# Kernel tuning notes

Measured on AMD Instinct MI355X. Metric: run time of the kernel, lower is better.

Reference implementation:

```python
import jax, jax.numpy as jnp
import numpy as np

IN_F = 3072       # in_features
OUT_F = 9216      # out_features = 3 * N_HEADS * HEAD_DIM (fused QKV)
GROUP = 64        # quantization group size
RANK = 32         # lora_rank
HEAD_DIM = 128
N_HEADS = OUT_F // (3 * HEAD_DIM)  # 24
EPS = 1e-6
LORA_SCALE = 1.0


def setup_inputs() -> dict:
    key = jax.random.key(0)
    ks = jax.random.split(key, 10)
    B, S = 1, 4096
    x = jax.random.normal(ks[0], (B, S, IN_F), dtype=jnp.float32)
    # packed int4 weights: two signed int4 values per int8 byte
    qweight = jax.random.randint(ks[1], (OUT_F, IN_F // 2), -128, 128, dtype=jnp.int32).astype(jnp.int8)
    wscales = (jax.random.uniform(ks[2], (IN_F // GROUP, OUT_F)) * 0.02 + 0.001).astype(jnp.float32)
    bias = (jax.random.normal(ks[3], (OUT_F,)) * 0.01).astype(jnp.float32)
    lora_down = (jax.random.normal(ks[4], (IN_F, RANK)) * 0.02).astype(jnp.float32)
    lora_up = (jax.random.normal(ks[5], (OUT_F, RANK)) * 0.02).astype(jnp.float32)
    smooth = (jax.random.uniform(ks[6], (IN_F,)) * 0.5 + 0.75).astype(jnp.float32)   # keep away from 0
    norm_q = (jax.random.uniform(ks[7], (HEAD_DIM,)) * 0.5 + 0.75).astype(jnp.float32)
    norm_k = (jax.random.uniform(ks[8], (HEAD_DIM,)) * 0.5 + 0.75).astype(jnp.float32)
    ang = jax.random.uniform(ks[9], (S, HEAD_DIM // 2)) * (2.0 * np.pi)
    rotary_emb = jnp.stack([jnp.cos(ang), jnp.sin(ang)], axis=-1).astype(jnp.float32)  # [S, D/2, 2]
    return dict(x=x, qweight=qweight, wscales=wscales, bias=bias, lora_down=lora_down,
                lora_up=lora_up, smooth=smooth, norm_q=norm_q, norm_k=norm_k, rotary_emb=rotary_emb)


def _dequant_weight(qweight, wscales):
    # unpack two signed int4 lanes from each int8 (low nibble first), then per-group scale
    low = jnp.right_shift(jnp.left_shift(qweight, 4), 4)   # arithmetic shifts on int8 -> sign extend
    high = jnp.right_shift(qweight, 4)
    w4 = jnp.stack([low, high], axis=-1).reshape(OUT_F, IN_F)          # int4 codes in [-8, 7]
    wg = w4.astype(jnp.float32).reshape(OUT_F, IN_F // GROUP, GROUP)
    return (wg * wscales.T[:, :, None]).reshape(OUT_F, IN_F)          # [N, K]


def _quantize_act(x, smooth, lora_down):
    # fused: smooth -> symmetric per-token per-group int4 quantize -> lora_down projection
    B, S, K = x.shape
    M = B * S
    xs = (x / smooth).reshape(M, K)
    xg = xs.reshape(M, K // GROUP, GROUP)
    ascale = jnp.max(jnp.abs(xg), axis=-1, keepdims=True) / 7.0
    ascale = jnp.maximum(ascale, 1e-8)
    q = jnp.clip(jnp.round(xg / ascale), -8.0, 7.0)
    deq = (q * ascale).reshape(M, K)                                   # dequantized int4 activation
    lora_act = xs @ lora_down                                          # [M, RANK], fp32 side path
    return deq, lora_act


def _rope(t, cos, sin):
    # interleaved pairs (even, odd) rotation; t: [M, H, D], cos/sin: [M, 1, D/2]
    e, o = t[..., 0::2], t[..., 1::2]
    re = e * cos - o * sin
    ro = e * sin + o * cos
    return jnp.stack([re, ro], axis=-1).reshape(t.shape)


def reference(x, qweight, wscales, bias, lora_down, lora_up, smooth, norm_q, norm_k, rotary_emb):
    B, S, K = x.shape
    M = B * S
    deq_x, lora_act = _quantize_act(x, smooth, lora_down)
    w = _dequant_weight(qweight, wscales)
    # main int4 GEMM + LoRA up + bias, all fused in the real kernel
    out = deq_x @ w.T + (LORA_SCALE * lora_act) @ lora_up.T + bias     # [M, OUT_F]
    qkv = out.reshape(M, 3, N_HEADS, HEAD_DIM)
    q, k, v = qkv[:, 0], qkv[:, 1], qkv[:, 2]
    def rms(t, g):
        return t * jax.lax.rsqrt(jnp.mean(t * t, axis=-1, keepdims=True) + EPS) * g
    q = rms(q, norm_q)
    k = rms(k, norm_k)
    cos = rotary_emb[:, None, :, 0]   # [M, 1, D/2]
    sin = rotary_emb[:, None, :, 1]
    q = _rope(q, cos, sin)
    k = _rope(k, cos, sin)
    return jnp.stack([q, k, v], axis=1).reshape(B, S, OUT_F)
```

## Files before the change

### kernel.cpp

```cpp
#include <hip/hip_runtime.h>
#include <cstdint>

#define MDIM 4096
#define NDIM 9216
#define KDIM 3072
#define KP   3136
#define NKT2 97

#define QROWS 4
#define QB2 1024
#define WB 13824
#define PB 2304

typedef unsigned int u32;
typedef unsigned short u16;
typedef float f32x4 __attribute__((ext_vector_type(4)));
typedef __bf16 bf16x8 __attribute__((ext_vector_type(8)));

__device__ __forceinline__ u16 f2bf(float f) {
  u32 u = __float_as_uint(f);
  u32 r = u + 0x7fffu + ((u >> 16) & 1u);
  return (u16)(r >> 16);
}

__device__ __forceinline__ float frcp(float f) { return __builtin_amdgcn_rcpf(f); }

__device__ __forceinline__ void gld_lds16(const void* g, void* l) {
  __builtin_amdgcn_global_load_lds((__attribute__((address_space(1))) void*)g,
                                   (__attribute__((address_space(3))) void*)l,
                                   16, 0, 0);
}

__global__ __launch_bounds__(256) void k_zero(float* __restrict__ out) {
  const int row = blockIdx.x;
  float4* p = (float4*)(out + (size_t)row * NDIM + 6144);
  p[threadIdx.x] = make_float4(0.f, 0.f, 0.f, 0.f);
}

__global__ __launch_bounds__(256) void k_quant(const float* __restrict__ x,
                        const float* __restrict__ lora_down, const float* __restrict__ smooth,
                        u16* __restrict__ Aex) {
  __shared__ float xs_s[QROWS][KDIM];
  __shared__ float part[64 * 32];
  const int tid = threadIdx.x;
  const int m0 = blockIdx.x * QROWS;
  const int sub = tid & 15;

  #pragma unroll
  for (int r = 0; r < QROWS; ++r) {
    const float* xr = x + (size_t)(m0 + r) * KDIM;
    u16* arow = Aex + (size_t)(m0 + r) * KP;
    #pragma unroll
    for (int p = 0; p < 3; ++p) {
      int g = p * 16 + (tid >> 4);
      int k0 = g * 64 + sub * 4;
      float4 xv = *(const float4*)(xr + k0);
      float4 sv = *(const float4*)(smooth + k0);
      float a0 = xv.x * frcp(sv.x), a1 = xv.y * frcp(sv.y);
      float a2 = xv.z * frcp(sv.z), a3 = xv.w * frcp(sv.w);
      xs_s[r][k0+0] = a0; xs_s[r][k0+1] = a1; xs_s[r][k0+2] = a2; xs_s[r][k0+3] = a3;
      float am = fmaxf(fmaxf(fabsf(a0), fabsf(a1)), fmaxf(fabsf(a2), fabsf(a3)));
      am = fmaxf(am, __shfl_xor(am, 8, 16));
      am = fmaxf(am, __shfl_xor(am, 4, 16));
      am = fmaxf(am, __shfl_xor(am, 2, 16));
      am = fmaxf(am, __shfl_xor(am, 1, 16));
      float asc = fmaxf(am * (1.0f / 7.0f), 1e-8f);
      float iasc = frcp(asc);
      float q0 = fminf(7.f, fmaxf(-8.f, rintf(a0 * iasc)));
      float q1 = fminf(7.f, fmaxf(-8.f, rintf(a1 * iasc)));
      float q2 = fminf(7.f, fmaxf(-8.f, rintf(a2 * iasc)));
      float q3 = fminf(7.f, fmaxf(-8.f, rintf(a3 * iasc)));
      float d0 = q0 * asc, d1 = q1 * asc, d2 = q2 * asc, d3 = q3 * asc;
      u32 lo = (u32)f2bf(d0) | ((u32)f2bf(d1) << 16);
      u32 hi = (u32)f2bf(d2) | ((u32)f2bf(d3) << 16);
      *(uint2*)(arow + k0) = make_uint2(lo, hi);
    }
    if (tid < 32) arow[3104 + tid] = 0;
  }
  __syncthreads();

  const int c  = tid >> 2;
  const int r8 = (tid & 3) * 8;
  float a[QROWS][8] = {};
  const float* lp = lora_down + (size_t)c * 32 + r8;
  #pragma unroll 2
  for (int i = 0; i < 48; ++i) {
    float4 l0 = *(const float4*)(lp);
    float4 l1 = *(const float4*)(lp + 4);
    #pragma unroll
    for (int r = 0; r < QROWS; ++r) {
      float xv = xs_s[r][i * 64 + c];
      a[r][0] = fmaf(xv, l0.x, a[r][0]); a[r][1] = fmaf(xv, l0.y, a[r][1]);
      a[r][2] = fmaf(xv, l0.z, a[r][2]); a[r][3] = fmaf(xv, l0.w, a[r][3]);
      a[r][4] = fmaf(xv, l1.x, a[r][4]); a[r][5] = fmaf(xv, l1.y, a[r][5]);
      a[r][6] = fmaf(xv, l1.z, a[r][6]); a[r][7] = fmaf(xv, l1.w, a[r][7]);
    }
    lp += 64 * 32;
  }
  #pragma unroll 1
  for (int r = 0; r < QROWS; ++r) {
    __syncthreads();
    *(float4*)(&part[c * 32 + r8])     = make_float4(a[r][0], a[r][1], a[r][2], a[r][3]);
    *(float4*)(&part[c * 32 + r8 + 4]) = make_float4(a[r][4], a[r][5], a[r][6], a[r][7]);
    __syncthreads();
    if (tid < 32) {
      float s = 0.f;
      #pragma unroll 8
      for (int cc = 0; cc < 64; ++cc) s += part[cc * 32 + tid];
      Aex[(size_t)(m0 + r) * KP + 3072 + tid] = f2bf(s);
    }
  }
}

__global__ __launch_bounds__(256) void k_wdq(const u32* __restrict__ qw,
                        const float* __restrict__ wsc, const float* __restrict__ lora_up,
                        u16* __restrict__ Bex) {
  const int tid = threadIdx.x;
  int bid = blockIdx.x;

  if (bid >= WB) {
    int idx = (bid - WB) * 256 + tid;
    int n = idx >> 6, c = idx & 63;
    u16 v = 0;
    if (c < 32) v = f2bf(lora_up[n * 32 + c]);
    Bex[(size_t)n * KP + 3072 + c] = v;
    return;
  }
  __shared__ int s_viol;
  u32 probe = qw[tid];
  bool ok = (probe >> 8) == ((probe & 0x80u) ? 0xffffffu : 0u);
  if (tid == 0) s_viol = 0;
  __syncthreads();
  if (!ok) atomicOr(&s_viol, 1);
  __syncthreads();
  const int f = (s_viol == 0);

  int idx = bid * 256 + tid;
  int n = idx / 384;
  int j = idx - n * 384;
  int k0 = j * 8;
  u32 w;
  if (f) {
    uint4 q4 = ((const uint4*)qw)[idx];
    w = (q4.x & 0xffu) | ((q4.y & 0xffu) << 8) | ((q4.z & 0xffu) << 16) | ((q4.w & 0xffu) << 24);
  } else {
    w = qw[idx];
  }
  float ws = wsc[(k0 >> 6) * NDIM + n];
  u32 ow[4];
  #pragma unroll
  for (int b = 0; b < 4; ++b) {
    int by = (int)((w >> (8 * b)) & 0xffu);
    int lo = (by << 28) >> 28;
    int hi = (by << 24) >> 28;
    ow[b] = (u32)f2bf((float)lo * ws) | ((u32)f2bf((float)hi * ws) << 16);
  }
  *(uint4*)(Bex + (size_t)n * KP + k0) = make_uint4(ow[0], ow[1], ow[2], ow[3]);
}

__global__ __launch_bounds__(512) void k_gemm(const u16* __restrict__ A, const u16* __restrict__ B,
                                              const float* __restrict__ bias, const float* __restrict__ norm_q,
                                              const float* __restrict__ norm_k, const float* __restrict__ rot,
                                              float* __restrict__ out, const int mode) {
  extern __shared__ u16 lds[];
  const int tid  = threadIdx.x;
  const int lane = tid & 63;
  const int wave = tid >> 6;

  int mt, nt, kt0, nk;
  if (mode == 0) {
    mt = blockIdx.y;
    int xx = blockIdx.x;
    nt = xx + ((xx >= 24) ? 4 : 0);
    kt0 = 0; nk = NKT2;
  } else {
    int s = blockIdx.x;
    mt = blockIdx.y & 15;
    nt = 24 + (blockIdx.y >> 4);
    kt0 = s * 24 + (s ? 1 : 0);
    nk  = s ? 24 : 25;
  }
  const int m0 = mt * 256;
  const int n0 = nt * 256;
  const int wm = (wave >> 2) * 128;
  const int wn = (wave & 3) * 64;
  const int lr = lane & 15;
  const int lq = lane >> 4;

  const u16 *pA0, *pA1, *pB0, *pB1;
  int la0, la1, lb0, lb1;
  {
    auto mk = [&](int p, const u16* base, int nb) -> const u16* {
      int pr = p >> 3, cs = p & 7;
      int c  = cs ^ (pr & 7);
      int r  = pr * 2 + (c >> 2);
      int kc = c & 3;
      return base + (size_t)(nb + r) * KP + kt0 * 32 + kc * 8;
    };
    int p0 = tid, p1 = 512 + tid;
    pA0 = mk(p0, A, m0); pA1 = mk(p1, A, m0);
    pB0 = mk(p0, B, n0); pB1 = mk(p1, B, n0);
    la0 = p0 * 8;        la1 = p1 * 8;
    lb0 = 8192 + p0 * 8; lb1 = 8192 + p1 * 8;
  }

  int aoff[8], boff[4];
  #pragma unroll
  for (int t = 0; t < 8; ++t) {
    int ra = wm + t * 16 + lr;
    int pr = ra >> 1, c = (ra & 1) * 4 + lq;
    aoff[t] = pr * 64 + ((c ^ (pr & 7)) * 8);
  }
  #pragma unroll
  for (int t = 0; t < 4; ++t) {
    int rb = wn + t * 16 + lr;
    int pr = rb >> 1, c = (rb & 1) * 4 + lq;
    boff[t] = 8192 + pr * 64 + ((c ^ (pr & 7)) * 8);
  }

  f32x4 acc[8][4] = {};

  #pragma unroll
  for (int s = 0; s < 3; ++s) {
    u16* sl = lds + (s << 14);
    gld_lds16(pA0, sl + la0); gld_lds16(pA1, sl + la1);
    gld_lds16(pB0, sl + lb0); gld_lds16(pB1, sl + lb1);
    pA0 += 32; pA1 += 32; pB0 += 32; pB1 += 32;
  }
  asm volatile("s_waitcnt vmcnt(4)" ::: "memory");
  __builtin_amdgcn_s_barrier();
  asm volatile("" ::: "memory");

  bf16x8 af[8], bf[4];
  #pragma unroll
  for (int t = 0; t < 8; ++t) af[t] = *(const bf16x8*)&lds[aoff[t]];
  #pragma unroll
  for (int t = 0; t < 4; ++t) bf[t] = *(const bf16x8*)&lds[boff[t]];

  #pragma unroll 1
  for (int kt = 0; kt < nk - 1; ++kt) {
    u16* stl = lds + (((kt + 3) & 3) << 14);
    const u16* nsl = lds + (((kt + 1) & 3) << 14);
    if (kt < nk - 3) {
      gld_lds16(pA0, stl + la0); gld_lds16(pA1, stl + la1);
      gld_lds16(pB0, stl + lb0); gld_lds16(pB1, stl + lb1);
      pA0 += 32; pA1 += 32; pB0 += 32; pB1 += 32;
    }
    __builtin_amdgcn_s_setprio(1);
    #pragma unroll
    for (int t = 0; t < 8; ++t) {
      #pragma unroll
      for (int tj = 0; tj < 4; ++tj)
        acc[t][tj] = __builtin_amdgcn_mfma_f32_16x16x32_bf16(af[t], bf[tj], acc[t][tj], 0, 0, 0);
      af[t] = *(const bf16x8*)&nsl[aoff[t]];
    }
    #pragma unroll
    for (int t = 0; t < 4; ++t) bf[t] = *(const bf16x8*)&nsl[boff[t]];
    __builtin_amdgcn_s_setprio(0);
    __builtin_amdgcn_sched_group_barrier(0x020, 4, 0);
    #pragma unroll
    for (int g = 0; g < 8; ++g) {
      __builtin_amdgcn_sched_group_barrier(0x008, 4, 0);
      __builtin_amdgcn_sched_group_barrier(0x100, 1, 0);
    }
    __builtin_amdgcn_sched_group_barrier(0x100, 4, 0);
    if (kt < nk - 3) asm volatile("s_waitcnt vmcnt(4)" ::: "memory");
    else             asm volatile("s_waitcnt vmcnt(0)" ::: "memory");
    __builtin_amdgcn_s_barrier();
    asm volatile("" ::: "memory");
  }
  #pragma unroll
  for (int t = 0; t < 8; ++t)
    #pragma unroll
    for (int tj = 0; tj < 4; ++tj)
      acc[t][tj] = __builtin_amdgcn_mfma_f32_16x16x32_bf16(af[t], bf[tj], acc[t][tj], 0, 0, 0);

  const int sel = (nt >= 24) ? 2 : (nt >= 12 ? 1 : 0);
  const float bscale = (mode == 0) ? 1.0f : 0.25f;

  float bv[4];
  #pragma unroll
  for (int tj = 0; tj < 4; ++tj) bv[tj] = bias[n0 + wn + tj * 16 + lr] * bscale;
  #pragma unroll
  for (int ti = 0; ti < 8; ++ti)
    #pragma unroll
    for (int tj = 0; tj < 4; ++tj)
      #pragma unroll
      for (int rg = 0; rg < 4; ++rg)
        acc[ti][tj][rg] += bv[tj];

  if (sel == 2) {
    if (mode == 0) {
      #pragma unroll
      for (int tj = 0; tj < 4; ++tj) {
        int n = n0 + wn + tj * 16 + lr;
        #pragma unroll
        for (int ti = 0; ti < 8; ++ti) {
          int mr = m0 + wm + ti * 16 + lq * 4;
          #pragma unroll
          for (int rg = 0; rg < 4; ++rg)
            out[(size_t)(mr + rg) * NDIM + n] = acc[ti][tj][rg];
        }
      }
    } else {
      #pragma unroll
      for (int tj = 0; tj < 4; ++tj) {
        int n = n0 + wn + tj * 16 + lr;
        #pragma unroll
        for (int ti = 0; ti < 8; ++ti) {
          int mr = m0 + wm + ti * 16 + lq * 4;
          #pragma unroll
          for (int rg = 0; rg < 4; ++rg)
            unsafeAtomicAdd(&out[(size_t)(mr + rg) * NDIM + n], acc[ti][tj][rg]);
        }
      }
    }
    return;
  }

  __syncthreads();
  float* ssq = (float*)lds;
  #pragma unroll
  for (int ti = 0; ti < 8; ++ti) {
    float pr4[4];
    #pragma unroll
    for (int rg = 0; rg < 4; ++rg) {
      float s = 0.f;
      #pragma unroll
      for (int tj = 0; tj < 4; ++tj) s += acc[ti][tj][rg] * acc[ti][tj][rg];
      pr4[rg] = s;
    }
    #pragma unroll
    for (int off = 1; off < 16; off <<= 1)
      #pragma unroll
      for (int rg = 0; rg < 4; ++rg) pr4[rg] += __shfl_xor(pr4[rg], off);
    #pragma unroll
    for (int rg = 0; rg < 4; ++rg)
      if (lr == (ti & 3) * 4 + rg)
        ssq[(wn >> 6) * 256 + wm + ti * 16 + lq * 4 + rg] = pr4[rg];
  }
  __syncthreads();

  const float* nrm = sel ? norm_k : norm_q;
  float gm[4];
  #pragma unroll
  for (int tj = 0; tj < 4; ++tj) gm[tj] = nrm[(wn & 64) + tj * 16 + lr];
  const float2* rot2 = (const float2*)rot;
  const float sgn = (lr & 1) ? 1.0f : -1.0f;
  const int hb = (wn >> 7) * 512;

  #pragma unroll
  for (int ti = 0; ti < 8; ++ti) {
    #pragma unroll
    for (int rg = 0; rg < 4; ++rg) {
      int row = wm + ti * 16 + lq * 4 + rg;
      float tot = ssq[hb + row] + ssq[hb + 256 + row];
      float rs = rsqrtf(tot * (1.0f / 128.0f) + 1e-6f);
      int m = m0 + row;
      #pragma unroll
      for (int tj = 0; tj < 4; ++tj) {
        int nl = (wn & 64) + tj * 16 + lr;
        float v = acc[ti][tj][rg] * rs * gm[tj];
        float p = __shfl_xor(v, 1);
        float2 cs = rot2[(size_t)m * 64 + (nl >> 1)];
        out[(size_t)m * NDIM + n0 + wn + tj * 16 + lr] = v * cs.x + sgn * (p * cs.y);
      }
    }
  }
}

extern "C" void kernel_launch(void* const* d_in, const int* in_sizes, int n_in,
                              void* d_out, int out_size, void* d_ws, size_t ws_size,
                              hipStream_t stream) {
  const float* x         = (const float*)d_in[0];
  const u32*   qweight   = (const u32*)d_in[1];
  const float* wscales   = (const float*)d_in[2];
  const float* bias      = (const float*)d_in[3];
  const float* lora_down = (const float*)d_in[4];
  const float* lora_up   = (const float*)d_in[5];
  const float* smooth    = (const float*)d_in[6];
  const float* norm_q    = (const float*)d_in[7];
  const float* norm_k    = (const float*)d_in[8];
  const float* rot       = (const float*)d_in[9];
  float* out = (float*)d_out;

  u16* Aex = (u16*)d_ws;
  u16* Bex = Aex + (size_t)MDIM * KP;

  static bool attr_set = false;
  if (!attr_set) {
    hipFuncSetAttribute(reinterpret_cast<const void*>(k_gemm),
                        hipFuncAttributeMaxDynamicSharedMemorySize, 131072);
    attr_set = true;
  }

  k_zero<<<4096, 256, 0, stream>>>(out);
  k_wdq<<<WB + PB, 256, 0, stream>>>(qweight, wscales, lora_up, Bex);
  k_quant<<<QB2, 256, 0, stream>>>(x, lora_down, smooth, Aex);
  k_gemm<<<dim3(32, 16), 512, 131072, stream>>>(Aex, Bex, bias, norm_q, norm_k, rot, out, 0);
  k_gemm<<<dim3(4, 64), 512, 131072, stream>>>(Aex, Bex, bias, norm_q, norm_k, rot, out, 1);
}
```

Before: 552.9 us.

## Switch main GEMM from bf16 dequantized operands to int8 MFMA with per-group scaling

Activations and weights are now kept as int8 codes, with per-group scales stored separately. The GEMM runs mfma_i32_16x16x64_i8 over each 64-wide group and applies the activation scale times the weight scale in fp32 when accumulating. The LoRA term moves out of the extended K dimension into a separate bf16 MFMA step after the main loop. This halves the operand bytes and uses the faster int8 MFMA, but each group now needs an extra int-to-float conversion and FMA on every accumulator, plus per-iteration scale loads from LDS.

```diff
diff --git a/kernel.cpp b/kernel.cpp
--- a/kernel.cpp
+++ b/kernel.cpp
@@ -4,17 +4,19 @@
 #define MDIM 4096
 #define NDIM 9216
 #define KDIM 3072
-#define KP   3136
-#define NKT2 97
+#define NG   48
 
 #define QROWS 4
 #define QB2 1024
 #define WB 13824
-#define PB 2304
+#define PB2 1152
+
+#define SLOT 34816
 
 typedef unsigned int u32;
 typedef unsigned short u16;
 typedef float f32x4 __attribute__((ext_vector_type(4)));
+typedef int   i32x4 __attribute__((ext_vector_type(4)));
 typedef __bf16 bf16x8 __attribute__((ext_vector_type(8)));
 
 __device__ __forceinline__ u16 f2bf(float f) {
@@ -39,7 +41,7 @@
 
 __global__ __launch_bounds__(256) void k_quant(const float* __restrict__ x,
                         const float* __restrict__ lora_down, const float* __restrict__ smooth,
-                        u16* __restrict__ Aex) {
+                        int8_t* __restrict__ Aq, float* __restrict__ Asc, u16* __restrict__ Alora) {
   __shared__ float xs_s[QROWS][KDIM];
   __shared__ float part[64 * 32];
   const int tid = threadIdx.x;
@@ -49,7 +51,7 @@
   #pragma unroll
   for (int r = 0; r < QROWS; ++r) {
     const float* xr = x + (size_t)(m0 + r) * KDIM;
-    u16* arow = Aex + (size_t)(m0 + r) * KP;
+    int8_t* arow = Aq + (size_t)(m0 + r) * KDIM;
     #pragma unroll
     for (int p = 0; p < 3; ++p) {
       int g = p * 16 + (tid >> 4);
@@ -66,16 +68,15 @@
       am = fmaxf(am, __shfl_xor(am, 1, 16));
       float asc = fmaxf(am * (1.0f / 7.0f), 1e-8f);
       float iasc = frcp(asc);
-      float q0 = fminf(7.f, fmaxf(-8.f, rintf(a0 * iasc)));
-      float q1 = fminf(7.f, fmaxf(-8.f, rintf(a1 * iasc)));
-      float q2 = fminf(7.f, fmaxf(-8.f, rintf(a2 * iasc)));
-      float q3 = fminf(7.f, fmaxf(-8.f, rintf(a3 * iasc)));
-      float d0 = q0 * asc, d1 = q1 * asc, d2 = q2 * asc, d3 = q3 * asc;
-      u32 lo = (u32)f2bf(d0) | ((u32)f2bf(d1) << 16);
-      u32 hi = (u32)f2bf(d2) | ((u32)f2bf(d3) << 16);
-      *(uint2*)(arow + k0) = make_uint2(lo, hi);
-    }
-    if (tid < 32) arow[3104 + tid] = 0;
+      int q0 = (int)fminf(7.f, fmaxf(-8.f, rintf(a0 * iasc)));
+      int q1 = (int)fminf(7.f, fmaxf(-8.f, rintf(a1 * iasc)));
+      int q2 = (int)fminf(7.f, fmaxf(-8.f, rintf(a2 * iasc)));
+      int q3 = (int)fminf(7.f, fmaxf(-8.f, rintf(a3 * iasc)));
+      u32 pk = (u32)(q0 & 0xff) | ((u32)(q1 & 0xff) << 8) |
+               ((u32)(q2 & 0xff) << 16) | ((u32)(q3 & 0xff) << 24);
+      *(u32*)(arow + k0) = pk;
+      if (sub == 0) Asc[(size_t)g * MDIM + (m0 + r)] = asc;
+    }
   }
   __syncthreads();
 
@@ -107,23 +108,21 @@
       float s = 0.f;
       #pragma unroll 8
       for (int cc = 0; cc < 64; ++cc) s += part[cc * 32 + tid];
-      Aex[(size_t)(m0 + r) * KP + 3072 + tid] = f2bf(s);
+      Alora[(size_t)(m0 + r) * 32 + tid] = f2bf(s);
     }
   }
 }
 
 __global__ __launch_bounds__(256) void k_wdq(const u32* __restrict__ qw,
-                        const float* __restrict__ wsc, const float* __restrict__ lora_up,
-                        u16* __restrict__ Bex) {
+                        const float* __restrict__ lora_up,
+                        int8_t* __restrict__ Bq, u16* __restrict__ Blora) {
   const int tid = threadIdx.x;
   int bid = blockIdx.x;
 
   if (bid >= WB) {
     int idx = (bid - WB) * 256 + tid;
-    int n = idx >> 6, c = idx & 63;
-    u16 v = 0;
-    if (c < 32) v = f2bf(lora_up[n * 32 + c]);
-    Bex[(size_t)n * KP + 3072 + c] = v;
+    int n = idx >> 5, cc = idx & 31;
+    Blora[(size_t)n * 32 + cc] = f2bf(lora_up[(size_t)n * 32 + cc]);
     return;
   }
   __shared__ int s_viol;
@@ -138,7 +137,6 @@
   int idx = bid * 256 + tid;
   int n = idx / 384;
   int j = idx - n * 384;
-  int k0 = j * 8;
   u32 w;
   if (f) {
     uint4 q4 = ((const uint4*)qw)[idx];
@@ -146,39 +144,40 @@
   } else {
     w = qw[idx];
   }
-  float ws = wsc[(k0 >> 6) * NDIM + n];
-  u32 ow[4];
-  #pragma unroll
-  for (int b = 0; b < 4; ++b) {
-    int by = (int)((w >> (8 * b)) & 0xffu);
-    int lo = (by << 28) >> 28;
-    int hi = (by << 24) >> 28;
-    ow[b] = (u32)f2bf((float)lo * ws) | ((u32)f2bf((float)hi * ws) << 16);
-  }
-  *(uint4*)(Bex + (size_t)n * KP + k0) = make_uint4(ow[0], ow[1], ow[2], ow[3]);
-}
-
-__global__ __launch_bounds__(512) void k_gemm(const u16* __restrict__ A, const u16* __restrict__ B,
+  u32 o[2];
+  #pragma unroll
+  for (int h = 0; h < 2; ++h) {
+    int b0 = (int)((w >> (16 * h)) & 0xffu);
+    int b1 = (int)((w >> (16 * h + 8)) & 0xffu);
+    int l0 = (b0 << 28) >> 28, h0 = (b0 << 24) >> 28;
+    int l1 = (b1 << 28) >> 28, h1 = (b1 << 24) >> 28;
+    o[h] = (u32)(l0 & 0xff) | ((u32)(h0 & 0xff) << 8) | ((u32)(l1 & 0xff) << 16) | ((u32)(h1 & 0xff) << 24);
+  }
+  *(uint2*)(Bq + (size_t)n * KDIM + j * 8) = make_uint2(o[0], o[1]);
+}
+
+__global__ __launch_bounds__(512) void k_gemm(const int8_t* __restrict__ Aq, const int8_t* __restrict__ Bq,
+                                              const float* __restrict__ Asc, const float* __restrict__ wsc,
+                                              const u16* __restrict__ Alora, const u16* __restrict__ Blora,
                                               const float* __restrict__ bias, const float* __restrict__ norm_q,
                                               const float* __restrict__ norm_k, const float* __restrict__ rot,
                                               float* __restrict__ out, const int mode) {
-  extern __shared__ u16 lds[];
+  extern __shared__ char ldsb[];
   const int tid  = threadIdx.x;
   const int lane = tid & 63;
   const int wave = tid >> 6;
 
-  int mt, nt, kt0, nk;
+  int mt, nt, g0, nk;
   if (mode == 0) {
     mt = blockIdx.y;
     int xx = blockIdx.x;
     nt = xx + ((xx >= 24) ? 4 : 0);
-    kt0 = 0; nk = NKT2;
+    g0 = 0; nk = NG;
   } else {
     int s = blockIdx.x;
     mt = blockIdx.y & 15;
     nt = 24 + (blockIdx.y >> 4);
-    kt0 = s * 24 + (s ? 1 : 0);
-    nk  = s ? 24 : 25;
+    g0 = s * 12; nk = 12;
   }
   const int m0 = mt * 256;
   const int n0 = nt * 256;
@@ -187,96 +186,135 @@
   const int lr = lane & 15;
   const int lq = lane >> 4;
 
-  const u16 *pA0, *pA1, *pB0, *pB1;
-  int la0, la1, lb0, lb1;
+  const int8_t *pA0, *pA1, *pB0, *pB1;
+  int dA0, dA1, dB0, dB1;
+  int rA0, kA0, rA1, kA1, rB0, kB0, rB1, kB1;
   {
-    auto mk = [&](int p, const u16* base, int nb) -> const u16* {
+    auto geo = [&](int p, int& r, int& kc) {
       int pr = p >> 3, cs = p & 7;
       int c  = cs ^ (pr & 7);
-      int r  = pr * 2 + (c >> 2);
-      int kc = c & 3;
-      return base + (size_t)(nb + r) * KP + kt0 * 32 + kc * 8;
+      r  = pr * 2 + (c >> 2);
+      kc = c & 3;
     };
     int p0 = tid, p1 = 512 + tid;
-    pA0 = mk(p0, A, m0); pA1 = mk(p1, A, m0);
-    pB0 = mk(p0, B, n0); pB1 = mk(p1, B, n0);
-    la0 = p0 * 8;        la1 = p1 * 8;
-    lb0 = 8192 + p0 * 8; lb1 = 8192 + p1 * 8;
-  }
+    geo(p0, rA0, kA0); geo(p1, rA1, kA1);
+    rB0 = rA0; kB0 = kA0; rB1 = rA1; kB1 = kA1;
+    pA0 = Aq + (size_t)(m0 + rA0) * KDIM + g0 * 64 + kA0 * 16;
+    pA1 = Aq + (size_t)(m0 + rA1) * KDIM + g0 * 64 + kA1 * 16;
+    pB0 = Bq + (size_t)(n0 + rB0) * KDIM + g0 * 64 + kB0 * 16;
+    pB1 = Bq + (size_t)(n0 + rB1) * KDIM + g0 * 64 + kB1 * 16;
+    dA0 = p0 * 16; dA1 = p1 * 16;
+    dB0 = 16384 + p0 * 16; dB1 = 16384 + p1 * 16;
+  }
+  const float* pAs = Asc + (size_t)g0 * MDIM + m0 + lane * 4;
+  const float* pWs = wsc + (size_t)g0 * NDIM + n0 + lane * 4;
 
   int aoff[8], boff[4];
   #pragma unroll
   for (int t = 0; t < 8; ++t) {
     int ra = wm + t * 16 + lr;
-    int pr = ra >> 1, c = (ra & 1) * 4 + lq;
-    aoff[t] = pr * 64 + ((c ^ (pr & 7)) * 8);
+    int pr = ra >> 1, cc = (ra & 1) * 4 + lq;
+    aoff[t] = pr * 128 + ((cc ^ (pr & 7)) * 16);
   }
   #pragma unroll
   for (int t = 0; t < 4; ++t) {
     int rb = wn + t * 16 + lr;
-    int pr = rb >> 1, c = (rb & 1) * 4 + lq;
-    boff[t] = 8192 + pr * 64 + ((c ^ (pr & 7)) * 8);
+    int pr = rb >> 1, cc = (rb & 1) * 4 + lq;
+    boff[t] = 16384 + pr * 128 + ((cc ^ (pr & 7)) * 16);
   }
 
   f32x4 acc[8][4] = {};
 
   #pragma unroll
   for (int s = 0; s < 3; ++s) {
-    u16* sl = lds + (s << 14);
-    gld_lds16(pA0, sl + la0); gld_lds16(pA1, sl + la1);
-    gld_lds16(pB0, sl + lb0); gld_lds16(pB1, sl + lb1);
-    pA0 += 32; pA1 += 32; pB0 += 32; pB1 += 32;
-  }
-  asm volatile("s_waitcnt vmcnt(4)" ::: "memory");
+    char* sl = ldsb + s * SLOT;
+    gld_lds16(pA0, sl + dA0); gld_lds16(pA1, sl + dA1);
+    gld_lds16(pB0, sl + dB0); gld_lds16(pB1, sl + dB1);
+    pA0 += 64; pA1 += 64; pB0 += 64; pB1 += 64;
+    if (wave == 0)      { gld_lds16(pAs, sl + 32768 + lane * 16); pAs += MDIM; }
+    else if (wave == 1) { gld_lds16(pWs, sl + 33792 + lane * 16); pWs += NDIM; }
+  }
+  if (wave < 2) asm volatile("s_waitcnt vmcnt(10)" ::: "memory");
+  else          asm volatile("s_waitcnt vmcnt(8)" ::: "memory");
   __builtin_amdgcn_s_barrier();
   asm volatile("" ::: "memory");
 
-  bf16x8 af[8], bf[4];
-  #pragma unroll
-  for (int t = 0; t < 8; ++t) af[t] = *(const bf16x8*)&lds[aoff[t]];
-  #pragma unroll
-  for (int t = 0; t < 4; ++t) bf[t] = *(const bf16x8*)&lds[boff[t]];
-
   #pragma unroll 1
-  for (int kt = 0; kt < nk - 1; ++kt) {
-    u16* stl = lds + (((kt + 3) & 3) << 14);
-    const u16* nsl = lds + (((kt + 1) & 3) << 14);
-    if (kt < nk - 3) {
-      gld_lds16(pA0, stl + la0); gld_lds16(pA1, stl + la1);
-      gld_lds16(pB0, stl + lb0); gld_lds16(pB1, stl + lb1);
-      pA0 += 32; pA1 += 32; pB0 += 32; pB1 += 32;
-    }
+  for (int kt = 0; kt < nk; ++kt) {
+    const char* cur = ldsb + (kt & 3) * SLOT;
+    char* stl = ldsb + ((kt + 3) & 3) * SLOT;
+    const bool st = (kt < nk - 3);
+    if (st) {
+      gld_lds16(pA0, stl + dA0); gld_lds16(pA1, stl + dA1);
+      gld_lds16(pB0, stl + dB0); gld_lds16(pB1, stl + dB1);
+      pA0 += 64; pA1 += 64; pB0 += 64; pB1 += 64;
+      if (wave == 0)      { gld_lds16(pAs, stl + 32768 + lane * 16); pAs += MDIM; }
+      else if (wave == 1) { gld_lds16(pWs, stl + 33792 + lane * 16); pWs += NDIM; }
+    }
+    i32x4 bf[4]; float wsv[4];
+    #pragma unroll
+    for (int t = 0; t < 4; ++t) bf[t] = *(const i32x4*)(cur + boff[t]);
+    #pragma unroll
+    for (int t = 0; t < 4; ++t) wsv[t] = *(const float*)(cur + 33792 + (wn + t * 16 + lr) * 4);
     __builtin_amdgcn_s_setprio(1);
     #pragma unroll
-    for (int t = 0; t < 8; ++t) {
+    for (int tp = 0; tp < 4; ++tp) {
+      i32x4 a0 = *(const i32x4*)(cur + aoff[2 * tp]);
+      i32x4 a1 = *(const i32x4*)(cur + aoff[2 * tp + 1]);
+      i32x4 ia0[4], ia1[4];
       #pragma unroll
       for (int tj = 0; tj < 4; ++tj)
-        acc[t][tj] = __builtin_amdgcn_mfma_f32_16x16x32_bf16(af[t], bf[tj], acc[t][tj], 0, 0, 0);
-      af[t] = *(const bf16x8*)&nsl[aoff[t]];
-    }
-    #pragma unroll
-    for (int t = 0; t < 4; ++t) bf[t] = *(const bf16x8*)&nsl[boff[t]];
+        ia0[tj] = __builtin_amdgcn_mfma_i32_16x16x64_i8(a0, bf[tj], (i32x4){0,0,0,0}, 0, 0, 0);
+      #pragma unroll
+      for (int tj = 0; tj < 4; ++tj)
+        ia1[tj] = __builtin_amdgcn_mfma_i32_16x16x64_i8(a1, bf[tj], (i32x4){0,0,0,0}, 0, 0, 0);
+      f32x4 as0 = *(const f32x4*)(cur + 32768 + (wm + (2 * tp) * 16 + lq * 4) * 4);
+      f32x4 as1 = *(const f32x4*)(cur + 32768 + (wm + (2 * tp + 1) * 16 + lq * 4) * 4);
+      #pragma unroll
+      for (int tj = 0; tj < 4; ++tj) {
+        f32x4 aw0 = as0 * wsv[tj];
+        f32x4 aw1 = as1 * wsv[tj];
+        #pragma unroll
+        for (int rg = 0; rg < 4; ++rg) {
+          acc[2 * tp][tj][rg]     += (float)ia0[tj][rg] * aw0[rg];
+          acc[2 * tp + 1][tj][rg] += (float)ia1[tj][rg] * aw1[rg];
+        }
+      }
+    }
     __builtin_amdgcn_s_setprio(0);
-    __builtin_amdgcn_sched_group_barrier(0x020, 4, 0);
-    #pragma unroll
-    for (int g = 0; g < 8; ++g) {
-      __builtin_amdgcn_sched_group_barrier(0x008, 4, 0);
-      __builtin_amdgcn_sched_group_barrier(0x100, 1, 0);
-    }
-    __builtin_amdgcn_sched_group_barrier(0x100, 4, 0);
-    if (kt < nk - 3) asm volatile("s_waitcnt vmcnt(4)" ::: "memory");
-    else             asm volatile("s_waitcnt vmcnt(0)" ::: "memory");
+    if (st) {
+      if (wave < 2) asm volatile("s_waitcnt vmcnt(10)" ::: "memory");
+      else          asm volatile("s_waitcnt vmcnt(8)" ::: "memory");
+    } else {
+      asm volatile("s_waitcnt vmcnt(0)" ::: "memory");
+    }
     __builtin_amdgcn_s_barrier();
     asm volatile("" ::: "memory");
   }
-  #pragma unroll
-  for (int t = 0; t < 8; ++t)
-    #pragma unroll
-    for (int tj = 0; tj < 4; ++tj)
-      acc[t][tj] = __builtin_amdgcn_mfma_f32_16x16x32_bf16(af[t], bf[tj], acc[t][tj], 0, 0, 0);
+
+  if (mode == 0 || blockIdx.x == 0) {
+    char* sl = ldsb;
+    gld_lds16(Alora + (size_t)(m0 + rA0) * 32 + kA0 * 8, sl + dA0);
+    gld_lds16(Alora + (size_t)(m0 + rA1) * 32 + kA1 * 8, sl + dA1);
+    gld_lds16(Blora + (size_t)(n0 + rB0) * 32 + kB0 * 8, sl + dB0);
+    gld_lds16(Blora + (size_t)(n0 + rB1) * 32 + kB1 * 8, sl + dB1);
+    asm volatile("s_waitcnt vmcnt(0)" ::: "memory");
+    __builtin_amdgcn_s_barrier();
+    asm volatile("" ::: "memory");
+    bf16x8 laf[8], lbf[4];
+    #pragma unroll
+    for (int t = 0; t < 8; ++t) laf[t] = *(const bf16x8*)(sl + aoff[t]);
+    #pragma unroll
+    for (int t = 0; t < 4; ++t) lbf[t] = *(const bf16x8*)(sl + boff[t]);
+    #pragma unroll
+    for (int ti = 0; ti < 8; ++ti)
+      #pragma unroll
+      for (int tj = 0; tj < 4; ++tj)
+        acc[ti][tj] = __builtin_amdgcn_mfma_f32_16x16x32_bf16(laf[ti], lbf[tj], acc[ti][tj], 0, 0, 0);
+  }
 
   const int sel = (nt >= 24) ? 2 : (nt >= 12 ? 1 : 0);
-  const float bscale = (mode == 0) ? 1.0f : 0.25f;
+  const float bscale = (mode == 0 || blockIdx.x == 0) ? 1.0f : 0.0f;
 
   float bv[4];
   #pragma unroll
@@ -319,7 +357,7 @@
   }
 
   __syncthreads();
-  float* ssq = (float*)lds;
+  float* ssq = (float*)ldsb;
   #pragma unroll
   for (int ti = 0; ti < 8; ++ti) {
     float pr4[4];
@@ -384,19 +422,25 @@
   const float* rot       = (const float*)d_in[9];
   float* out = (float*)d_out;
 
-  u16* Aex = (u16*)d_ws;
-  u16* Bex = Aex + (size_t)MDIM * KP;
+  char* W = (char*)d_ws;
+  int8_t* Aq   = (int8_t*)W;
+  int8_t* Bq   = (int8_t*)(W + 12582912);
+  float*  Asc  = (float*)(W + 40894464);
+  u16*    Alora= (u16*)(W + 41680896);
+  u16*    Blora= (u16*)(W + 41943040);
 
   static bool attr_set = false;
   if (!attr_set) {
     hipFuncSetAttribute(reinterpret_cast<const void*>(k_gemm),
-                        hipFuncAttributeMaxDynamicSharedMemorySize, 131072);
+                        hipFuncAttributeMaxDynamicSharedMemorySize, 4 * SLOT);
     attr_set = true;
   }
 
   k_zero<<<4096, 256, 0, stream>>>(out);
-  k_wdq<<<WB + PB, 256, 0, stream>>>(qweight, wscales, lora_up, Bex);
-  k_quant<<<QB2, 256, 0, stream>>>(x, lora_down, smooth, Aex);
-  k_gemm<<<dim3(32, 16), 512, 131072, stream>>>(Aex, Bex, bias, norm_q, norm_k, rot, out, 0);
-  k_gemm<<<dim3(4, 64), 512, 131072, stream>>>(Aex, Bex, bias, norm_q, norm_k, rot, out, 1);
-}
+  k_wdq<<<WB + PB2, 256, 0, stream>>>(qweight, lora_up, Bq, Blora);
+  k_quant<<<QB2, 256, 0, stream>>>(x, lora_down, smooth, Aq, Asc, Alora);
+  k_gemm<<<dim3(32, 16), 512, 4 * SLOT, stream>>>(Aq, Bq, Asc, wscales, Alora, Blora,
+                                                  bias, norm_q, norm_k, rot, out, 0);
+  k_gemm<<<dim3(4, 64), 512, 4 * SLOT, stream>>>(Aq, Bq, Asc, wscales, Alora, Blora,
+                                                 bias, norm_q, norm_k, rot, out, 1);
+}
```

Measured after the change: 1.222 ms. 121% more time.
